# Kernel optimization log

Hardware: AMD Instinct MI355X
Metric: run time of the kernel (lower is better)

Reference implementation:

```python
import jax, jax.numpy as jnp
import numpy as np
from jax import lax

B, DIM, H, DM, NH = 32, 16, 128, 256, 8  # batch, in-channels, seq, d_model, n_head


def setup_inputs() -> dict:
    key = jax.random.key(0)
    k1, k2, k3, k4, k5 = jax.random.split(key, 5)
    x = jax.random.normal(k1, (B, DIM, H, DM), jnp.float32)
    conv1_w = jax.random.normal(k2, (3 * NH * DIM, 1, 5, 1), jnp.float32) * 0.1
    conv2_w = jax.random.normal(k3, (3 * NH * DIM, 1, 1, NH), jnp.float32) * 0.1
    w_out_w = jax.random.normal(k4, (DM, DM), jnp.float32) * (1.0 / np.sqrt(DM))
    w_out_b = jax.random.normal(k5, (DM,), jnp.float32) * 0.01
    return dict(x=x, conv1_w=conv1_w, conv2_w=conv2_w, w_out_w=w_out_w, w_out_b=w_out_b)


def reference(x, conv1_w, conv2_w, w_out_w, w_out_b):
    b, dim, h, w = x.shape
    nh = conv2_w.shape[-1]
    dn = ('NCHW', 'OIHW', 'NCHW')
    # grouped conv (5,1), padding 'same' on height, groups=dim
    y = lax.conv_general_dilated(x, conv1_w, (1, 1), [(2, 2), (0, 0)],
                                 dimension_numbers=dn, feature_group_count=dim)
    # depthwise conv (1, nh) stride (1, nh): width w -> w/nh
    y = lax.conv_general_dilated(y, conv2_w, (1, nh), [(0, 0), (0, 0)],
                                 dimension_numbers=dn, feature_group_count=y.shape[1])
    # dropout layers are identity in eval mode
    C = nh * dim
    wp = w // nh
    y = y.reshape(b, 3, C, h, wp)  # 'b (n c) h w -> n b c h w' split, n=3 outer
    q, k, v = y[:, 0], y[:, 1], y[:, 2]  # each [b, C, h, wp]
    scores = jnp.einsum('bcqd,bckd->bcqk', q, k) / jnp.sqrt(jnp.float32(wp))
    attn = jax.nn.softmax(scores, axis=-1)
    o = jnp.einsum('bcqk,bckd->bcqd', attn, v)  # [b, C, h, wp]
    # 'b (c n) h w -> b c h (n w)' with c=dim, n=nh
    o = o.reshape(b, dim, nh, h, wp).transpose(0, 1, 3, 2, 4).reshape(b, dim, h, nh * wp)
    return o @ w_out_w.T + w_out_b
```

## Files before the change

### kernel.cpp

```cpp
#include <hip/hip_runtime.h>
#include <stdint.h>

#define B_   32
#define DIM_ 16
#define H_   128
#define DM_  256
#define NH_  8
#define WP_  32
#define C3_  384

typedef short bf16x8 __attribute__((ext_vector_type(8)));
typedef float f32x4  __attribute__((ext_vector_type(4)));

__device__ __forceinline__ unsigned short f2bfu(float v) {
    unsigned int x = __float_as_uint(v);
    x += 0x7fffu + ((x >> 16) & 1u);
    return (unsigned short)(x >> 16);
}
__device__ __forceinline__ unsigned cvtpk(float lo, float hi) {
    unsigned r;
    asm("v_cvt_pk_bf16_f32 %0, %1, %2" : "=v"(r) : "v"(lo), "v"(hi));
    return r;
}
__device__ __forceinline__ void gl_lds16(const void* g, void* l) {
    __builtin_amdgcn_global_load_lds(
        (const __attribute__((address_space(1))) unsigned int*)g,
        (__attribute__((address_space(3))) unsigned int*)l, 16, 0, 0);
}

__global__ __launch_bounds__(256) void conv_kernel(
    const float* __restrict__ x, const float* __restrict__ w1,
    const float* __restrict__ w2, unsigned short* __restrict__ y2)
{
    const int bid = blockIdx.x;
    const int ht = bid & 1;
    const int g  = (bid >> 1) & 15;
    const int b  = bid >> 5;
    const int tid = threadIdx.x;
    const int wp = tid & 31;
    const int hl = tid >> 5;
    const int h0 = ht * 64 + hl * 8;

    const float* xbase = x + ((size_t)(b * DIM_ + g) * H_) * DM_ + wp * 8;

    float xr[12][8];
    #pragma unroll
    for (int r = 0; r < 12; ++r) {
        const int hr = h0 - 2 + r;
        if (hr >= 0 && hr < H_) {
            const float4* p = (const float4*)(xbase + (size_t)hr * DM_);
            float4 a = p[0], c = p[1];
            xr[r][0] = a.x; xr[r][1] = a.y; xr[r][2] = a.z; xr[r][3] = a.w;
            xr[r][4] = c.x; xr[r][5] = c.y; xr[r][6] = c.z; xr[r][7] = c.w;
        } else {
            #pragma unroll
            for (int j = 0; j < 8; ++j) xr[r][j] = 0.f;
        }
    }

    unsigned short* yb = y2 + (((size_t)(b * C3_ + g * 24)) * H_ + h0) * WP_ + wp;

    for (int oc = 0; oc < 24; ++oc) {
        const int o = g * 24 + oc;
        const float* pw1 = w1 + o * 5;
        const float* pw2 = w2 + o * 8;
        float w1r[5], w2r[8];
        #pragma unroll
        for (int t = 0; t < 5; ++t) w1r[t] = pw1[t];
        #pragma unroll
        for (int j = 0; j < 8; ++j) w2r[j] = pw2[j];

        float u[12];
        #pragma unroll
        for (int r = 0; r < 12; ++r) {
            float s = w2r[0] * xr[r][0];
            #pragma unroll
            for (int j = 1; j < 8; ++j) s = fmaf(w2r[j], xr[r][j], s);
            u[r] = s;
        }

        #pragma unroll
        for (int hh = 0; hh < 8; ++hh) {
            float yv = w1r[0] * u[hh];
            #pragma unroll
            for (int t = 1; t < 5; ++t) yv = fmaf(w1r[t], u[hh + t], yv);
            yb[(size_t)oc * (H_ * WP_) + hh * WP_] = f2bfu(yv);
        }
    }
}

__global__ __launch_bounds__(256) void attn_kernel(
    const unsigned short* __restrict__ y2, unsigned short* __restrict__ z)
{
    __shared__ __align__(16) unsigned char sm[40960];

    const int tid = threadIdx.x;
    const int ch = blockIdx.x & 127, b = blockIdx.x >> 7;
    const size_t base = ((size_t)(b * C3_ + ch)) * 4096;
    const uint4* qg = (const uint4*)(y2 + base);
    const uint4* kg = (const uint4*)(y2 + base + 128 * 4096);
    const uint4* vg = (const uint4*)(y2 + base + 256 * 4096);

    #pragma unroll
    for (int r = 0; r < 2; ++r) {
        const int ci  = tid + r * 256;
        const int row = ci >> 2;
        const int c   = ci & 3;
        const int cx  = c ^ ((row >> 1) & 3);
        *(uint4*)(sm + row * 64 + cx * 16)        = qg[ci];
        *(uint4*)(sm + 8192 + row * 64 + cx * 16) = kg[ci];
        uint4 v = vg[ci];
        unsigned short vs[8];
        vs[0] = (unsigned short)(v.x & 0xffffu); vs[1] = (unsigned short)(v.x >> 16);
        vs[2] = (unsigned short)(v.y & 0xffffu); vs[3] = (unsigned short)(v.y >> 16);
        vs[4] = (unsigned short)(v.z & 0xffffu); vs[5] = (unsigned short)(v.z >> 16);
        vs[6] = (unsigned short)(v.w & 0xffffu); vs[7] = (unsigned short)(v.w >> 16);
        const int d0 = c * 8;
        #pragma unroll
        for (int j = 0; j < 8; ++j) {
            const int d = d0 + j;
            *(unsigned short*)(sm + 32768 + d * 256 + ((row * 2) ^ ((d & 7) << 4))) = vs[j];
        }
    }
    __syncthreads();

    const int l  = tid & 63, wv = tid >> 6;
    const int lm = l & 15,  lk = l >> 4;

    bf16x8 qf[2];
    #pragma unroll
    for (int t = 0; t < 2; ++t) {
        const int q = (wv * 2 + t) * 16 + lm;
        qf[t] = *(const bf16x8*)(sm + q * 64 + ((lk ^ ((q >> 1) & 3)) << 4));
    }
    f32x4 acc[8][2];
    #pragma unroll
    for (int rt = 0; rt < 8; ++rt) {
        acc[rt][0] = 0; acc[rt][1] = 0;
    }
    #pragma unroll
    for (int rt = 0; rt < 8; ++rt) {
        const int kr = rt * 16 + lm;
        bf16x8 kf = *(const bf16x8*)(sm + 8192 + kr * 64 + ((lk ^ ((kr >> 1) & 3)) << 4));
        acc[rt][0] = __builtin_amdgcn_mfma_f32_16x16x32_bf16(kf, qf[0], acc[rt][0], 0, 0, 0);
        acc[rt][1] = __builtin_amdgcn_mfma_f32_16x16x32_bf16(kf, qf[1], acc[rt][1], 0, 0, 0);
    }

    const float Cc = 0.17677669529663687f * 1.4426950408889634f;
    float inv[2];
    #pragma unroll
    for (int t = 0; t < 2; ++t) {
        float m = acc[0][t][0];
        #pragma unroll
        for (int rt = 0; rt < 8; ++rt)
            #pragma unroll
            for (int rg = 0; rg < 4; ++rg) m = fmaxf(m, acc[rt][t][rg]);
        m = fmaxf(m, __shfl_xor(m, 16));
        m = fmaxf(m, __shfl_xor(m, 32));
        float s = 0.f;
        #pragma unroll
        for (int rt = 0; rt < 8; ++rt)
            #pragma unroll
            for (int rg = 0; rg < 4; ++rg) {
                float p = exp2f((acc[rt][t][rg] - m) * Cc);
                acc[rt][t][rg] = p; s += p;
            }
        s += __shfl_xor(s, 16);
        s += __shfl_xor(s, 32);
        inv[t] = 1.0f / s;
    }

    __syncthreads();

    #pragma unroll
    for (int t = 0; t < 2; ++t) {
        const int q = (wv * 2 + t) * 16 + lm;
        #pragma unroll
        for (int rt = 0; rt < 8; ++rt) {
            unsigned u0 = cvtpk(acc[rt][t][0] * inv[t], acc[rt][t][1] * inv[t]);
            unsigned u1 = cvtpk(acc[rt][t][2] * inv[t], acc[rt][t][3] * inv[t]);
            const int kb = rt * 32 + lk * 8;
            *(uint2*)(sm + q * 256 + (kb ^ ((q & 7) << 4))) = make_uint2(u0, u1);
        }
    }
    __syncthreads();

    f32x4 o[2][2];
    o[0][0] = 0; o[0][1] = 0; o[1][0] = 0; o[1][1] = 0;
    #pragma unroll
    for (int kc = 0; kc < 4; ++kc) {
        const int cb = kc * 64 + lk * 16;
        bf16x8 av[2], bp[2];
        #pragma unroll
        for (int dt = 0; dt < 2; ++dt) {
            const int d = dt * 16 + lm;
            av[dt] = *(const bf16x8*)(sm + 32768 + d * 256 + (cb ^ ((d & 7) << 4)));
        }
        #pragma unroll
        for (int t = 0; t < 2; ++t) {
            const int q = (wv * 2 + t) * 16 + lm;
            bp[t] = *(const bf16x8*)(sm + q * 256 + (cb ^ ((q & 7) << 4)));
        }
        #pragma unroll
        for (int dt = 0; dt < 2; ++dt)
            #pragma unroll
            for (int t = 0; t < 2; ++t)
                o[dt][t] = __builtin_amdgcn_mfma_f32_16x16x32_bf16(av[dt], bp[t], o[dt][t], 0, 0, 0);
    }

    const int dd = ch >> 3, nn = ch & 7;
    unsigned short* zb = z + ((size_t)(b * DIM_ + dd)) * (H_ * DM_);
    #pragma unroll
    for (int dt = 0; dt < 2; ++dt)
        #pragma unroll
        for (int t = 0; t < 2; ++t) {
            const int q  = (wv * 2 + t) * 16 + lm;
            const int d0 = dt * 16 + lk * 4;
            unsigned u0 = cvtpk(o[dt][t][0], o[dt][t][1]);
            unsigned u1 = cvtpk(o[dt][t][2], o[dt][t][3]);
            *(uint2*)(zb + (size_t)q * DM_ + nn * 32 + d0) = make_uint2(u0, u1);
        }
}

__global__ __launch_bounds__(256) void prep_w(
    const float* __restrict__ w, unsigned short* __restrict__ wh,
    unsigned short* __restrict__ wl)
{
    const int i = blockIdx.x * 1024 + threadIdx.x * 4;
    float4 v = *(const float4*)(w + i);
    float vv[4] = { v.x, v.y, v.z, v.w };
    unsigned short h[4], lo[4];
    #pragma unroll
    for (int j = 0; j < 4; ++j) {
        h[j] = f2bfu(vv[j]);
        float hf = __uint_as_float(((unsigned)h[j]) << 16);
        lo[j] = f2bfu(vv[j] - hf);
    }
    *(uint2*)(wh + i) = make_uint2((unsigned)h[0] | ((unsigned)h[1] << 16),
                                   (unsigned)h[2] | ((unsigned)h[3] << 16));
    *(uint2*)(wl + i) = make_uint2((unsigned)lo[0] | ((unsigned)lo[1] << 16),
                                   (unsigned)lo[2] | ((unsigned)lo[3] << 16));
}

__global__ __launch_bounds__(256) void proj_kernel(
    const unsigned short* __restrict__ zz, const unsigned short* __restrict__ wh,
    const unsigned short* __restrict__ wl, const float* __restrict__ bias,
    float* __restrict__ out)
{
    __shared__ __align__(16) unsigned char sm[65536];
    const int tid = threadIdx.x;
    const int l = tid & 63, wv = tid >> 6, lm = l & 15, lk = l >> 4;
    const unsigned short* zs = zz + (size_t)blockIdx.x * 32768;

    const int g_off = (tid >> 2) * 256 + (tid & 3) * 8;
    const int lds_wv = wv * 1024;

    const int arow0 = wv * 32 + lm;

    f32x4 acc[2][16];
    #pragma unroll
    for (int t = 0; t < 2; ++t)
        #pragma unroll
        for (int nt = 0; nt < 16; ++nt) acc[t][nt] = 0;

    bf16x8 areg[2][2];

    #pragma unroll
    for (int i = 0; i < 8; ++i) {
        const unsigned short* g = (i < 4 ? wh : wl) + g_off + (i & 3) * 16384;
        gl_lds16(g, sm + i * 4096 + lds_wv);
    }
    #pragma unroll
    for (int t = 0; t < 2; ++t)
        areg[0][t] = *(const bf16x8*)(zs + (size_t)(arow0 + t * 16) * 256 + lk * 8);

    __syncthreads();

    #pragma unroll
    for (int kc = 0; kc < 8; ++kc) {
        const int buf = kc & 1;
        if (kc < 7) {
            #pragma unroll
            for (int i = 0; i < 8; ++i) {
                const unsigned short* g = (i < 4 ? wh : wl) + g_off + (i & 3) * 16384 + (kc + 1) * 32;
                gl_lds16(g, sm + (buf ^ 1) * 32768 + i * 4096 + lds_wv);
            }
            #pragma unroll
            for (int t = 0; t < 2; ++t)
                areg[buf ^ 1][t] = *(const bf16x8*)(zs + (size_t)(arow0 + t * 16) * 256 + (kc + 1) * 32 + lk * 8);
        }
        #pragma unroll
        for (int ph = 0; ph < 2; ++ph)
            #pragma unroll
            for (int nt = 0; nt < 16; ++nt) {
                bf16x8 bf = *(const bf16x8*)(sm + buf * 32768 + ph * 16384 + nt * 1024 + lm * 64 + lk * 16);
                acc[0][nt] = __builtin_amdgcn_mfma_f32_16x16x32_bf16(areg[buf][0], bf, acc[0][nt], 0, 0, 0);
                acc[1][nt] = __builtin_amdgcn_mfma_f32_16x16x32_bf16(areg[buf][1], bf, acc[1][nt], 0, 0, 0);
            }
        __syncthreads();
    }

    float* ob = out + (size_t)blockIdx.x * 32768;
    #pragma unroll
    for (int t = 0; t < 2; ++t)
        #pragma unroll
        for (int nt = 0; nt < 16; ++nt) {
            const float bv = bias[nt * 16 + lm];
            #pragma unroll
            for (int rg = 0; rg < 4; ++rg)
                ob[(size_t)(wv * 32 + t * 16 + lk * 4 + rg) * 256 + nt * 16 + lm] = acc[t][nt][rg] + bv;
        }
}

extern "C" void kernel_launch(void* const* d_in, const int* in_sizes, int n_in,
                              void* d_out, int out_size, void* d_ws, size_t ws_size,
                              hipStream_t stream)
{
    const float* x  = (const float*)d_in[0];
    const float* w1 = (const float*)d_in[1];
    const float* w2 = (const float*)d_in[2];
    const float* wo = (const float*)d_in[3];
    const float* wb = (const float*)d_in[4];
    float* out = (float*)d_out;

    unsigned short* y2 = (unsigned short*)d_ws;
    unsigned short* zz = y2 + (size_t)B_ * C3_ * H_ * WP_;
    unsigned short* wh = y2;
    unsigned short* wl = y2 + 65536;

    conv_kernel<<<dim3(1024), dim3(256), 0, stream>>>(x, w1, w2, y2);
    attn_kernel<<<dim3(4096), dim3(256), 0, stream>>>(y2, zz);
    prep_w<<<dim3(64), dim3(256), 0, stream>>>(wo, wh, wl);
    proj_kernel<<<dim3(512), dim3(256), 0, stream>>>(zz, wh, wl, wb, out);
}
```

Measured before the change: 122.6 us.

## Recast grouped conv as MFMA GEMM with split-bf16 input and vectorize output stores

```diff
diff --git a/kernel.cpp b/kernel.cpp
--- a/kernel.cpp
+++ b/kernel.cpp
@@ -32,60 +32,93 @@
     const float* __restrict__ x, const float* __restrict__ w1,
     const float* __restrict__ w2, unsigned short* __restrict__ y2)
 {
+    __shared__ __align__(16) unsigned char sm[77824];
+
     const int bid = blockIdx.x;
     const int ht = bid & 1;
     const int g  = (bid >> 1) & 15;
     const int b  = bid >> 5;
     const int tid = threadIdx.x;
-    const int wp = tid & 31;
-    const int hl = tid >> 5;
-    const int h0 = ht * 64 + hl * 8;
-
-    const float* xbase = x + ((size_t)(b * DIM_ + g) * H_) * DM_ + wp * 8;
-
-    float xr[12][8];
-    #pragma unroll
-    for (int r = 0; r < 12; ++r) {
-        const int hr = h0 - 2 + r;
-        if (hr >= 0 && hr < H_) {
-            const float4* p = (const float4*)(xbase + (size_t)hr * DM_);
-            float4 a = p[0], c = p[1];
-            xr[r][0] = a.x; xr[r][1] = a.y; xr[r][2] = a.z; xr[r][3] = a.w;
-            xr[r][4] = c.x; xr[r][5] = c.y; xr[r][6] = c.z; xr[r][7] = c.w;
-        } else {
-            #pragma unroll
-            for (int j = 0; j < 8; ++j) xr[r][j] = 0.f;
-        }
-    }
-
-    unsigned short* yb = y2 + (((size_t)(b * C3_ + g * 24)) * H_ + h0) * WP_ + wp;
-
-    for (int oc = 0; oc < 24; ++oc) {
-        const int o = g * 24 + oc;
-        const float* pw1 = w1 + o * 5;
-        const float* pw2 = w2 + o * 8;
-        float w1r[5], w2r[8];
-        #pragma unroll
-        for (int t = 0; t < 5; ++t) w1r[t] = pw1[t];
-        #pragma unroll
-        for (int j = 0; j < 8; ++j) w2r[j] = pw2[j];
-
-        float u[12];
-        #pragma unroll
-        for (int r = 0; r < 12; ++r) {
-            float s = w2r[0] * xr[r][0];
-            #pragma unroll
-            for (int j = 1; j < 8; ++j) s = fmaf(w2r[j], xr[r][j], s);
-            u[r] = s;
-        }
-
-        #pragma unroll
-        for (int hh = 0; hh < 8; ++hh) {
-            float yv = w1r[0] * u[hh];
-            #pragma unroll
-            for (int t = 1; t < 5; ++t) yv = fmaf(w1r[t], u[hh + t], yv);
-            yb[(size_t)oc * (H_ * WP_) + hh * WP_] = f2bfu(yv);
-        }
+
+    const float* xg = x + ((size_t)(b * DIM_ + g)) * H_ * DM_;
+
+    for (int i = tid; i < 2240; i += 256) {
+        const int row = i >> 5, c = i & 31;
+        const int hg = ht * 64 + row - 2;
+        float4 fa = make_float4(0.f, 0.f, 0.f, 0.f);
+        float4 fb = make_float4(0.f, 0.f, 0.f, 0.f);
+        if (hg >= 0 && hg < H_) {
+            const float4* p = (const float4*)(xg + (size_t)hg * DM_ + c * 8);
+            fa = p[0]; fb = p[1];
+        }
+        unsigned h0 = cvtpk(fa.x, fa.y), h1 = cvtpk(fa.z, fa.w);
+        unsigned h2 = cvtpk(fb.x, fb.y), h3 = cvtpk(fb.z, fb.w);
+        unsigned l0 = cvtpk(fa.x - __uint_as_float(h0 << 16),
+                            fa.y - __uint_as_float(h0 & 0xffff0000u));
+        unsigned l1 = cvtpk(fa.z - __uint_as_float(h1 << 16),
+                            fa.w - __uint_as_float(h1 & 0xffff0000u));
+        unsigned l2 = cvtpk(fb.x - __uint_as_float(h2 << 16),
+                            fb.y - __uint_as_float(h2 & 0xffff0000u));
+        unsigned l3 = cvtpk(fb.z - __uint_as_float(h3 << 16),
+                            fb.w - __uint_as_float(h3 & 0xffff0000u));
+        const int off = row * 512 + ((c ^ (row & 7)) << 4);
+        *(uint4*)(sm + off)         = make_uint4(h0, h1, h2, h3);
+        *(uint4*)(sm + 35840 + off) = make_uint4(l0, l1, l2, l3);
+    }
+
+    unsigned short* smW = (unsigned short*)(sm + 71680);
+    for (int i = tid; i < 3072; i += 256) {
+        const int o = i / 96, k = i % 96;
+        const int kk = (k >= 48) ? k - 48 : k;
+        const int t = kk >> 3, j = kk & 7;
+        float w = 0.f;
+        if (o < 24 && t < 5)
+            w = w1[(g * 24 + o) * 5 + t] * w2[(g * 24 + o) * 8 + j];
+        smW[o * 96 + k] = f2bfu(w);
+    }
+    __syncthreads();
+
+    const int l = tid & 63, wv = tid >> 6, lm = l & 15, lk = l >> 4;
+
+    bf16x8 aw[2][3];
+    #pragma unroll
+    for (int mt = 0; mt < 2; ++mt)
+        #pragma unroll
+        for (int kf = 0; kf < 3; ++kf)
+            aw[mt][kf] = *(const bf16x8*)((const unsigned char*)smW
+                          + (mt * 16 + lm) * 192 + kf * 64 + lk * 16);
+
+    int tpar[3], ppar[3];
+    #pragma unroll
+    for (int kf = 0; kf < 3; ++kf) {
+        const int k0 = kf * 32 + lk * 8;
+        const int part = (k0 >= 48) ? 1 : 0;
+        tpar[kf] = (k0 - part * 48) >> 3;
+        ppar[kf] = part * 35840;
+    }
+
+    unsigned short* zb = y2 + (size_t)(b * C3_ + g * 24) * 4096;
+
+    for (int i = 0; i < 32; ++i) {
+        const int nt = wv * 32 + i;
+        const int h_l = nt >> 1, wpb = (nt & 1) << 4;
+        const int wp = wpb + lm;
+        f32x4 acc0 = 0, acc1 = 0;
+        #pragma unroll
+        for (int kf = 0; kf < 3; ++kf) {
+            const int rl = h_l + tpar[kf];
+            bf16x8 xb = *(const bf16x8*)(sm + ppar[kf] + rl * 512
+                          + ((wp ^ (rl & 7)) << 4));
+            acc0 = __builtin_amdgcn_mfma_f32_16x16x32_bf16(xb, aw[0][kf], acc0, 0, 0, 0);
+            acc1 = __builtin_amdgcn_mfma_f32_16x16x32_bf16(xb, aw[1][kf], acc1, 0, 0, 0);
+        }
+        const int h = ht * 64 + h_l;
+        const int wpst = wpb + lk * 4;
+        *(uint2*)(zb + (size_t)lm * 4096 + h * 32 + wpst) =
+            make_uint2(cvtpk(acc0[0], acc0[1]), cvtpk(acc0[2], acc0[3]));
+        if (lm < 8)
+            *(uint2*)(zb + (size_t)(16 + lm) * 4096 + h * 32 + wpst) =
+                make_uint2(cvtpk(acc1[0], acc1[1]), cvtpk(acc1[2], acc1[3]));
     }
 }
 
@@ -294,22 +327,25 @@
             #pragma unroll
             for (int nt = 0; nt < 16; ++nt) {
                 bf16x8 bf = *(const bf16x8*)(sm + buf * 32768 + ph * 16384 + nt * 1024 + lm * 64 + lk * 16);
-                acc[0][nt] = __builtin_amdgcn_mfma_f32_16x16x32_bf16(areg[buf][0], bf, acc[0][nt], 0, 0, 0);
-                acc[1][nt] = __builtin_amdgcn_mfma_f32_16x16x32_bf16(areg[buf][1], bf, acc[1][nt], 0, 0, 0);
+                acc[0][nt] = __builtin_amdgcn_mfma_f32_16x16x32_bf16(bf, areg[buf][0], acc[0][nt], 0, 0, 0);
+                acc[1][nt] = __builtin_amdgcn_mfma_f32_16x16x32_bf16(bf, areg[buf][1], acc[1][nt], 0, 0, 0);
             }
         __syncthreads();
     }
 
     float* ob = out + (size_t)blockIdx.x * 32768;
     #pragma unroll
-    for (int t = 0; t < 2; ++t)
+    for (int t = 0; t < 2; ++t) {
+        const int row = wv * 32 + t * 16 + lm;
         #pragma unroll
         for (int nt = 0; nt < 16; ++nt) {
-            const float bv = bias[nt * 16 + lm];
-            #pragma unroll
-            for (int rg = 0; rg < 4; ++rg)
-                ob[(size_t)(wv * 32 + t * 16 + lk * 4 + rg) * 256 + nt * 16 + lm] = acc[t][nt][rg] + bv;
-        }
+            const int col = nt * 16 + lk * 4;
+            const float4 bv = *(const float4*)(bias + col);
+            float4 vv = make_float4(acc[t][nt][0] + bv.x, acc[t][nt][1] + bv.y,
+                                    acc[t][nt][2] + bv.z, acc[t][nt][3] + bv.w);
+            *(float4*)&ob[(size_t)row * 256 + col] = vv;
+        }
+    }
 }
 
 extern "C" void kernel_launch(void* const* d_in, const int* in_sizes, int n_in,
```

Result: faster. 119.4 us (-2.6%).
